# Kernel tuning notes

Hardware: AMD Instinct MI355X
Metric: run time of the kernel (lower is better)

The kernel has to match this reference:

```python
import jax, jax.numpy as jnp
import numpy as np

B, T, D = 2, 1024, 1024
H, DK = 16, 64  # n_head, d_k; inner dim = H*DK = D
INV_SQRT_DK = 1.0 / float(np.sqrt(DK))


def setup_inputs() -> dict:
    key = jax.random.key(0)
    ks = jax.random.split(key, 16)
    init = lambda k, shape: (jax.random.normal(k, shape, dtype=jnp.float32) * 0.02)
    return {
        "query": jax.random.normal(ks[0], (B, T, D), dtype=jnp.float32),
        "key": jax.random.normal(ks[1], (B, T, D), dtype=jnp.float32),
        "value": jax.random.normal(ks[2], (B, T, D), dtype=jnp.float32),
        "pos_k": jax.random.normal(ks[3], (T, T, DK), dtype=jnp.float32),
        "pos_v": jax.random.normal(ks[4], (T, T, DK), dtype=jnp.float32),
        "mask": jnp.ones((B, T, T), dtype=jnp.int32),
        "relative_attention_bias": jax.random.normal(ks[5], (1, H, T, T), dtype=jnp.float32),
        "Wq": init(ks[6], (D, D)), "bq": init(ks[7], (D,)),
        "Wk": init(ks[8], (D, D)), "bk": init(ks[9], (D,)),
        "Wv": init(ks[10], (D, D)), "bv": init(ks[11], (D,)),
        "Wo": init(ks[12], (D, D)), "bo": init(ks[13], (D,)),
    }


def reference(query, key, value, pos_k, pos_v, mask, relative_attention_bias,
              Wq, bq, Wk, bk, Wv, bv, Wo, bo):
    nb = query.shape[0]
    # projections -> (B, H, T, DK); q pre-scaled by 1/sqrt(d_k)
    q = (query @ Wq + bq).reshape(nb, -1, H, DK).transpose(0, 2, 1, 3) * INV_SQRT_DK
    k = (key @ Wk + bk).reshape(nb, -1, H, DK).transpose(0, 2, 1, 3)
    v = (value @ Wv + bv).reshape(nb, -1, H, DK).transpose(0, 2, 1, 3)

    # content scores + relative-position key scores (B, H, T, S)
    A = jnp.einsum('bhtd,bhsd->bhts', q, k)
    Bp = jnp.einsum('bhtd,tsd->bhts', q, pos_k)
    scores = A + Bp + relative_attention_bias

    # masked softmax: mask (B, T, S) -> invalid where mask == 0
    inv = (mask[:, None, :, :] == 0)  # (B, 1, T, S)
    scores = jnp.where(inv, -jnp.inf, scores)
    attn = jax.nn.softmax(scores, axis=-1)
    attn = jnp.where(inv, 0.0, attn)

    # value aggregation + relative-position value term
    x = jnp.einsum('bhts,bhsd->bhtd', attn, v)
    x = x + jnp.einsum('bhts,tsd->bhtd', attn, pos_v)

    x = x.transpose(0, 2, 1, 3).reshape(nb, -1, H * DK)  # (B, T, D)
    return x @ Wo + bo
```

## Files before the change

kernel.cpp:

```cpp
#include <hip/hip_runtime.h>


#define DEV __device__ __forceinline__

typedef short bf16x8 __attribute__((ext_vector_type(8)));
typedef float f32x4 __attribute__((ext_vector_type(4)));

DEV short f2b(float f) {
  unsigned u = __builtin_bit_cast(unsigned, f);
  u = (u + 0x7FFFu + ((u >> 16) & 1u)) >> 16;
  return (short)u;
}
DEV float b2f(short s) {
  unsigned u = ((unsigned)(unsigned short)s) << 16;
  return __builtin_bit_cast(float, u);
}

#define MFMA(a, b, c) __builtin_amdgcn_mfma_f32_16x16x32_bf16(a, b, c, 0, 0, 0)

__global__ __launch_bounds__(256) void k_cvt3(
    const float* __restrict__ a, const float* __restrict__ b, const float* __restrict__ c,
    short* __restrict__ oa, short* __restrict__ ob, short* __restrict__ oc) {
  const float* src = blockIdx.y == 0 ? a : (blockIdx.y == 1 ? b : c);
  short* dst = blockIdx.y == 0 ? oa : (blockIdx.y == 1 ? ob : oc);
  size_t i = ((size_t)blockIdx.x * 256 + threadIdx.x) * 8;
  float4 p0 = *(const float4*)(src + i);
  float4 p1 = *(const float4*)(src + i + 4);
  bf16x8 o;
  o[0] = f2b(p0.x); o[1] = f2b(p0.y); o[2] = f2b(p0.z); o[3] = f2b(p0.w);
  o[4] = f2b(p1.x); o[5] = f2b(p1.y); o[6] = f2b(p1.z); o[7] = f2b(p1.w);
  *(bf16x8*)(dst + i) = o;
}

__global__ __launch_bounds__(256) void k_wtrans4(
    const float* __restrict__ w0, const float* __restrict__ w1,
    const float* __restrict__ w2, const float* __restrict__ w3,
    short* __restrict__ o0, short* __restrict__ o1,
    short* __restrict__ o2, short* __restrict__ o3) {
  const float* src; short* dst;
  switch (blockIdx.z) {
    case 0: src = w0; dst = o0; break;
    case 1: src = w1; dst = o1; break;
    case 2: src = w2; dst = o2; break;
    default: src = w3; dst = o3;
  }
  __shared__ short LW[64][74];
  const int tid = threadIdx.x;
  const int k0 = blockIdx.y * 64, n0 = blockIdx.x * 64;
  {
    int c4 = (tid & 15) * 4;
#pragma unroll
    for (int i = 0; i < 4; ++i) {
      int r = (tid >> 4) + i * 16;
      float4 v = *(const float4*)(src + (size_t)(k0 + r) * 1024 + n0 + c4);
      LW[r][c4 + 0] = f2b(v.x); LW[r][c4 + 1] = f2b(v.y);
      LW[r][c4 + 2] = f2b(v.z); LW[r][c4 + 3] = f2b(v.w);
    }
  }
  __syncthreads();
  {
    int n = tid >> 2, kb = (tid & 3) * 16;
#pragma unroll
    for (int j2 = 0; j2 < 2; ++j2) {
      int kk = kb + j2 * 8;
      bf16x8 o;
#pragma unroll
      for (int j = 0; j < 8; ++j) o[j] = LW[kk + j][n];
      *(bf16x8*)(dst + (size_t)(n0 + n) * 1024 + k0 + kk) = o;
    }
  }
}

__global__ __launch_bounds__(256) void k_proj(
    const short* __restrict__ A, const short* __restrict__ WT,
    const float* __restrict__ bias, short* __restrict__ out, float scale) {
  __shared__ short As[64][40];
  __shared__ short Bs[64][40];
  const int n0 = blockIdx.x * 64, m0 = blockIdx.y * 64;
  const int tid = threadIdx.x;
  const int w = tid >> 6, l = tid & 63, lg = l >> 4, lr = l & 15;
  const int wm = (w >> 1) * 2, wn = (w & 1) * 2;
  const int sr = tid >> 2, sc = (tid & 3) * 8;
  f32x4 acc[2][2] = {};
  for (int k0 = 0; k0 < 1024; k0 += 32) {
    *(bf16x8*)&As[sr][sc] = *(const bf16x8*)(A + (size_t)(m0 + sr) * 1024 + k0 + sc);
    *(bf16x8*)&Bs[sr][sc] = *(const bf16x8*)(WT + (size_t)(n0 + sr) * 1024 + k0 + sc);
    __syncthreads();
    bf16x8 af[2], bfr[2];
#pragma unroll
    for (int mi = 0; mi < 2; ++mi) af[mi] = *(const bf16x8*)&As[(wm + mi) * 16 + lr][lg * 8];
#pragma unroll
    for (int ni = 0; ni < 2; ++ni) bfr[ni] = *(const bf16x8*)&Bs[(wn + ni) * 16 + lr][lg * 8];
#pragma unroll
    for (int mi = 0; mi < 2; ++mi)
#pragma unroll
      for (int ni = 0; ni < 2; ++ni) acc[mi][ni] = MFMA(af[mi], bfr[ni], acc[mi][ni]);
    __syncthreads();
  }
#pragma unroll
  for (int mi = 0; mi < 2; ++mi)
#pragma unroll
    for (int ni = 0; ni < 2; ++ni)
#pragma unroll
      for (int r = 0; r < 4; ++r) {
        int m = m0 + (wm + mi) * 16 + lg * 4 + r;
        int n = n0 + (wn + ni) * 16 + lr;
        float val = (acc[mi][ni][r] + bias[n]) * scale;
        int b = m >> 10, t = m & 1023, h = n >> 6, dk = n & 63;
        out[((size_t)(b * 16 + h) * 1024 + t) * 64 + dk] = f2b(val);
      }
}

__global__ __launch_bounds__(256) void k_projT(
    const short* __restrict__ A, const short* __restrict__ WT,
    const float* __restrict__ bias, short* __restrict__ out) {
  __shared__ short As[64][40];
  __shared__ short Bs[64][40];
  const int n0 = blockIdx.x * 64, m0 = blockIdx.y * 64;
  const int tid = threadIdx.x;
  const int w = tid >> 6, l = tid & 63, lg = l >> 4, lr = l & 15;
  const int wm = (w >> 1) * 2, wn = (w & 1) * 2;
  const int sr = tid >> 2, sc = (tid & 3) * 8;
  f32x4 acc[2][2] = {};
  for (int k0 = 0; k0 < 1024; k0 += 32) {
    *(bf16x8*)&As[sr][sc] = *(const bf16x8*)(A + (size_t)(m0 + sr) * 1024 + k0 + sc);
    *(bf16x8*)&Bs[sr][sc] = *(const bf16x8*)(WT + (size_t)(n0 + sr) * 1024 + k0 + sc);
    __syncthreads();
    bf16x8 af[2], bfr[2];
#pragma unroll
    for (int mi = 0; mi < 2; ++mi) af[mi] = *(const bf16x8*)&As[(wm + mi) * 16 + lr][lg * 8];
#pragma unroll
    for (int ni = 0; ni < 2; ++ni) bfr[ni] = *(const bf16x8*)&Bs[(wn + ni) * 16 + lr][lg * 8];
#pragma unroll
    for (int mi = 0; mi < 2; ++mi)
#pragma unroll
      for (int ni = 0; ni < 2; ++ni) acc[mi][ni] = MFMA(af[mi], bfr[ni], acc[mi][ni]);
    __syncthreads();
  }
#pragma unroll
  for (int mi = 0; mi < 2; ++mi)
#pragma unroll
    for (int ni = 0; ni < 2; ++ni)
#pragma unroll
      for (int r = 0; r < 4; ++r) {
        int m = m0 + (wm + mi) * 16 + lg * 4 + r;
        int n = n0 + (wn + ni) * 16 + lr;
        float val = acc[mi][ni][r] + bias[n];
        int b = m >> 10, t = m & 1023, h = n >> 6, dk = n & 63;
        out[(((size_t)(b * 16 + h) * 64 + dk) << 10) + t] = f2b(val);
      }
}

__global__ __launch_bounds__(256) void k_posk_bias(
    const short* __restrict__ q, const float* __restrict__ pos_k,
    const float* __restrict__ rab, const int* __restrict__ mask,
    short* __restrict__ S) {
  const int t = blockIdx.y;
  const int tid = threadIdx.x;
  const int w = tid >> 6, l = tid & 63, lg = l >> 4, lr = l & 15;
  const int s0 = blockIdx.x * 256 + w * 64;
  __shared__ short LW[4][32][74];
  bf16x8 af[2][2];
#pragma unroll
  for (int mi = 0; mi < 2; ++mi)
#pragma unroll
    for (int kk = 0; kk < 2; ++kk) {
      int bh = mi * 16 + lr;
      af[mi][kk] = *(const bf16x8*)(q + ((size_t)bh * 1024 + t) * 64 + kk * 32 + lg * 8);
    }
  f32x4 acc[2][4] = {};
#pragma unroll
  for (int ni = 0; ni < 4; ++ni) {
    int s = s0 + ni * 16 + lr;
#pragma unroll
    for (int kk = 0; kk < 2; ++kk) {
      const float* pk = pos_k + ((size_t)t * 1024 + s) * 64 + kk * 32 + lg * 8;
      const float4 p0 = *(const float4*)pk;
      const float4 p1 = *(const float4*)(pk + 4);
      bf16x8 bfr;
      bfr[0] = f2b(p0.x); bfr[1] = f2b(p0.y); bfr[2] = f2b(p0.z); bfr[3] = f2b(p0.w);
      bfr[4] = f2b(p1.x); bfr[5] = f2b(p1.y); bfr[6] = f2b(p1.z); bfr[7] = f2b(p1.w);
#pragma unroll
      for (int mi = 0; mi < 2; ++mi) acc[mi][ni] = MFMA(af[mi][kk], bfr, acc[mi][ni]);
    }
  }
#pragma unroll
  for (int ni = 0; ni < 4; ++ni) {
    int s = s0 + ni * 16 + lr;
    int msk0 = mask[(size_t)t * 1024 + s];
    int msk1 = mask[(size_t)(1024 + t) * 1024 + s];
#pragma unroll
    for (int r = 0; r < 4; ++r) {
      int h = lg * 4 + r;
      float bv = rab[((size_t)h * 1024 + t) * 1024 + s];
      float v0 = acc[0][ni][r] + bv;
      float v1 = acc[1][ni][r] + bv;
      if (msk0 == 0) v0 = -1e30f;
      if (msk1 == 0) v1 = -1e30f;
      LW[w][h][ni * 16 + lr] = f2b(v0);
      LW[w][16 + h][ni * 16 + lr] = f2b(v1);
    }
  }
#pragma unroll
  for (int rr = 0; rr < 4; ++rr) {
    int row = (l >> 3) + rr * 8;
    int s8 = (l & 7) * 8;
    bf16x8 o = *(const bf16x8*)&LW[w][row][s8];
    *(bf16x8*)(S + ((size_t)row * 1024 + t) * 1024 + s0 + s8) = o;
  }
}

__global__ __launch_bounds__(512, 4) void k_attn_softmax(
    const short* __restrict__ q, const short* __restrict__ kmat,
    short* __restrict__ S) {
  const int bh = blockIdx.y;
  const int tid = threadIdx.x;
  const int w = tid >> 6, l = tid & 63, lg = l >> 4, lr = l & 15;
  const int wm = w >> 2, wn = w & 3;
  const int t0 = blockIdx.x * 32 + wm * 16;
  const int scol = wn * 256;
  __shared__ short LS[8][16][266];
  __shared__ float redA[32][4];
  __shared__ float redB[32][4];

  short* sb = (short*)(S + ((size_t)bh * 1024 + t0) * 1024 + scol);
  const int r2 = l >> 5, c16 = (l & 31) * 8;
#pragma unroll
  for (int rr = 0; rr < 8; ++rr) {
    int row = rr * 2 + r2;
    *(bf16x8*)&LS[w][row][c16] = *(const bf16x8*)(sb + (size_t)row * 1024 + c16);
  }

  bf16x8 af[2];
#pragma unroll
  for (int kk = 0; kk < 2; ++kk)
    af[kk] = *(const bf16x8*)(q + ((size_t)bh * 1024 + (t0 + lr)) * 64 + kk * 32 + lg * 8);

  f32x4 acc[16];
#pragma unroll
  for (int ni = 0; ni < 16; ++ni) {
    int s = scol + ni * 16 + lr;
    const short* kp = kmat + ((size_t)bh * 1024 + s) * 64 + lg * 8;
    bf16x8 b0 = *(const bf16x8*)kp;
    bf16x8 b1 = *(const bf16x8*)(kp + 32);
    f32x4 a = {};
    a = MFMA(af[0], b0, a);
    a = MFMA(af[1], b1, a);
    acc[ni] = a;
  }
#pragma unroll
  for (int ni = 0; ni < 16; ++ni)
#pragma unroll
    for (int r = 0; r < 4; ++r) acc[ni][r] += b2f(LS[w][lg * 4 + r][ni * 16 + lr]);

  float pm[4];
#pragma unroll
  for (int r = 0; r < 4; ++r) {
    float m = acc[0][r];
#pragma unroll
    for (int ni = 1; ni < 16; ++ni) m = fmaxf(m, acc[ni][r]);
    m = fmaxf(m, __shfl_xor(m, 1));
    m = fmaxf(m, __shfl_xor(m, 2));
    m = fmaxf(m, __shfl_xor(m, 4));
    m = fmaxf(m, __shfl_xor(m, 8));
    pm[r] = m;
  }
  if (lr == 0) {
#pragma unroll
    for (int r = 0; r < 4; ++r) redA[wm * 16 + lg * 4 + r][wn] = pm[r];
  }
  __syncthreads();
  float rowm[4];
#pragma unroll
  for (int r = 0; r < 4; ++r) {
    int row = wm * 16 + lg * 4 + r;
    rowm[r] = fmaxf(fmaxf(redA[row][0], redA[row][1]), fmaxf(redA[row][2], redA[row][3]));
  }
  float rs[4];
#pragma unroll
  for (int r = 0; r < 4; ++r) {
    float sum = 0.f;
#pragma unroll
    for (int ni = 0; ni < 16; ++ni) {
      float e = __expf(acc[ni][r] - rowm[r]);
      acc[ni][r] = e;
      sum += e;
    }
    sum += __shfl_xor(sum, 1);
    sum += __shfl_xor(sum, 2);
    sum += __shfl_xor(sum, 4);
    sum += __shfl_xor(sum, 8);
    rs[r] = sum;
  }
  if (lr == 0) {
#pragma unroll
    for (int r = 0; r < 4; ++r) redB[wm * 16 + lg * 4 + r][wn] = rs[r];
  }
  __syncthreads();
#pragma unroll
  for (int r = 0; r < 4; ++r) {
    int row = wm * 16 + lg * 4 + r;
    float inv = 1.0f / (redB[row][0] + redB[row][1] + redB[row][2] + redB[row][3]);
#pragma unroll
    for (int ni = 0; ni < 16; ++ni) LS[w][lg * 4 + r][ni * 16 + lr] = f2b(acc[ni][r] * inv);
  }
#pragma unroll
  for (int rr = 0; rr < 8; ++rr) {
    int row = rr * 2 + r2;
    bf16x8 o = *(const bf16x8*)&LS[w][row][c16];
    *(bf16x8*)(sb + (size_t)row * 1024 + c16) = o;
  }
}

__global__ __launch_bounds__(256) void k_posv(
    const short* __restrict__ S, const float* __restrict__ pos_v,
    short* __restrict__ X0h) {
  const int t = blockIdx.x;
  const int tid = threadIdx.x;
  const int w = tid >> 6, l = tid & 63, lg = l >> 4, lr = l & 15;
  const int mi = w >> 1;
  const int nb = (w & 1) * 2;
  __shared__ short pv[256][66];
  f32x4 acc[2] = {};
  const int srow = tid >> 4;
  const int dk4 = (tid & 15) * 4;
  for (int c = 0; c < 4; ++c) {
    int sc = c * 256;
    if (c) __syncthreads();
#pragma unroll
    for (int it = 0; it < 16; ++it) {
      int s = srow + it * 16;
      float4 p = *(const float4*)(pos_v + ((size_t)t * 1024 + sc + s) * 64 + dk4);
      unsigned p0 = (unsigned)(unsigned short)f2b(p.x) | ((unsigned)(unsigned short)f2b(p.y) << 16);
      unsigned p1 = (unsigned)(unsigned short)f2b(p.z) | ((unsigned)(unsigned short)f2b(p.w) << 16);
      *(unsigned*)&pv[s][dk4] = p0;
      *(unsigned*)&pv[s][dk4 + 2] = p1;
    }
    __syncthreads();
    const int bh = mi * 16 + lr;
#pragma unroll
    for (int kk = 0; kk < 8; ++kk) {
      bf16x8 afr = *(const bf16x8*)(S + ((size_t)bh * 1024 + t) * 1024 + sc + kk * 32 + lg * 8);
#pragma unroll
      for (int ni = 0; ni < 2; ++ni) {
        int dk = (nb + ni) * 16 + lr;
        bf16x8 bfr;
#pragma unroll
        for (int j = 0; j < 8; ++j) bfr[j] = pv[kk * 32 + lg * 8 + j][dk];
        acc[ni] = MFMA(afr, bfr, acc[ni]);
      }
    }
  }
#pragma unroll
  for (int ni = 0; ni < 2; ++ni)
#pragma unroll
    for (int r = 0; r < 4; ++r) {
      int bh = mi * 16 + lg * 4 + r;
      int b = bh >> 4, h = bh & 15;
      int dk = (nb + ni) * 16 + lr;
      X0h[((size_t)(b * 1024 + t)) * 1024 + h * 64 + dk] = f2b(acc[ni][r]);
    }
}

__global__ __launch_bounds__(256) void k_av(
    const short* __restrict__ S, const short* __restrict__ vT,
    const short* __restrict__ X0h, short* __restrict__ X) {
  const int bh = blockIdx.y;
  const int tt0 = blockIdx.x * 128;
  const int tid = threadIdx.x;
  const int w = tid >> 6, l = tid & 63, lg = l >> 4, lr = l & 15;
  const short* vbase = vT + ((size_t)bh << 16);
  const short* sbase = S + ((size_t)bh << 20);
  f32x4 acc[2][4] = {};
#pragma unroll 4
  for (int kk = 0; kk < 32; ++kk) {
    bf16x8 afr[2];
#pragma unroll
    for (int mi = 0; mi < 2; ++mi) {
      int tt = tt0 + (w * 2 + mi) * 16 + lr;
      afr[mi] = *(const bf16x8*)(sbase + ((size_t)tt << 10) + kk * 32 + lg * 8);
    }
#pragma unroll
    for (int ni = 0; ni < 4; ++ni) {
      bf16x8 bfr = *(const bf16x8*)(vbase + ((ni * 16 + lr) << 10) + kk * 32 + lg * 8);
#pragma unroll
      for (int mi = 0; mi < 2; ++mi) acc[mi][ni] = MFMA(afr[mi], bfr, acc[mi][ni]);
    }
  }
  const int b = bh >> 4, h = bh & 15;
#pragma unroll
  for (int mi = 0; mi < 2; ++mi)
#pragma unroll
    for (int ni = 0; ni < 4; ++ni)
#pragma unroll
      for (int r = 0; r < 4; ++r) {
        int tt = tt0 + (w * 2 + mi) * 16 + lg * 4 + r;
        int d = h * 64 + ni * 16 + lr;
        size_t idx = ((size_t)(b * 1024 + tt)) * 1024 + d;
        X[idx] = f2b(b2f(X0h[idx]) + acc[mi][ni][r]);
      }
}

__global__ __launch_bounds__(256) void k_oproj(
    const short* __restrict__ X, const short* __restrict__ WT,
    const float* __restrict__ bias, float* __restrict__ out) {
  __shared__ short As[64][40];
  __shared__ short Bs[64][40];
  const int n0 = blockIdx.x * 64, m0 = blockIdx.y * 64;
  const int tid = threadIdx.x;
  const int w = tid >> 6, l = tid & 63, lg = l >> 4, lr = l & 15;
  const int wm = (w >> 1) * 2, wn = (w & 1) * 2;
  const int sr = tid >> 2, sc = (tid & 3) * 8;
  f32x4 acc[2][2] = {};
  for (int k0 = 0; k0 < 1024; k0 += 32) {
    *(bf16x8*)&As[sr][sc] = *(const bf16x8*)(X + (size_t)(m0 + sr) * 1024 + k0 + sc);
    *(bf16x8*)&Bs[sr][sc] = *(const bf16x8*)(WT + (size_t)(n0 + sr) * 1024 + k0 + sc);
    __syncthreads();
    bf16x8 af[2], bfr[2];
#pragma unroll
    for (int mi = 0; mi < 2; ++mi) af[mi] = *(const bf16x8*)&As[(wm + mi) * 16 + lr][lg * 8];
#pragma unroll
    for (int ni = 0; ni < 2; ++ni) bfr[ni] = *(const bf16x8*)&Bs[(wn + ni) * 16 + lr][lg * 8];
#pragma unroll
    for (int mi = 0; mi < 2; ++mi)
#pragma unroll
      for (int ni = 0; ni < 2; ++ni) acc[mi][ni] = MFMA(af[mi], bfr[ni], acc[mi][ni]);
    __syncthreads();
  }
#pragma unroll
  for (int mi = 0; mi < 2; ++mi)
#pragma unroll
    for (int ni = 0; ni < 2; ++ni)
#pragma unroll
      for (int r = 0; r < 4; ++r) {
        int m = m0 + (wm + mi) * 16 + lg * 4 + r;
        int n = n0 + (wn + ni) * 16 + lr;
        out[(size_t)m * 1024 + n] = acc[mi][ni][r] + bias[n];
      }
}

extern "C" void kernel_launch(void* const* d_in, const int* in_sizes, int n_in,
                              void* d_out, int out_size, void* d_ws, size_t ws_size,
                              hipStream_t stream) {
  (void)in_sizes; (void)n_in; (void)out_size; (void)ws_size;
  const float* query = (const float*)d_in[0];
  const float* key   = (const float*)d_in[1];
  const float* value = (const float*)d_in[2];
  const float* pos_k = (const float*)d_in[3];
  const float* pos_v = (const float*)d_in[4];
  const int*   mask  = (const int*)d_in[5];
  const float* rab   = (const float*)d_in[6];
  const float* Wq = (const float*)d_in[7];
  const float* bq = (const float*)d_in[8];
  const float* Wk = (const float*)d_in[9];
  const float* bk = (const float*)d_in[10];
  const float* Wv = (const float*)d_in[11];
  const float* bv = (const float*)d_in[12];
  const float* Wo = (const float*)d_in[13];
  const float* bo = (const float*)d_in[14];
  float* out = (float*)d_out;

  const size_t M2 = 2ull * 1024 * 1024;
  short* q   = (short*)d_ws;
  short* k   = q + M2;
  short* vT  = k + M2;
  short* S   = vT + M2;
  short* X0h = S + 32ull * 1024 * 1024;
  short* X   = X0h + M2;
  short* qin = X + M2;
  short* kin = qin + M2;
  short* vin = kin + M2;
  short* WqT = vin + M2;
  short* WkT = WqT + 1024 * 1024;
  short* WvT = WkT + 1024 * 1024;
  short* WoT = WvT + 1024 * 1024;

  k_cvt3<<<dim3(1024, 3), dim3(256), 0, stream>>>(query, key, value, qin, kin, vin);
  k_wtrans4<<<dim3(16, 16, 4), dim3(256), 0, stream>>>(Wq, Wk, Wv, Wo, WqT, WkT, WvT, WoT);
  k_proj<<<dim3(16, 32), dim3(256), 0, stream>>>(qin, WqT, bq, q, 0.125f);
  k_proj<<<dim3(16, 32), dim3(256), 0, stream>>>(kin, WkT, bk, k, 1.0f);
  k_projT<<<dim3(16, 32), dim3(256), 0, stream>>>(vin, WvT, bv, vT);
  k_posk_bias<<<dim3(4, 1024), dim3(256), 0, stream>>>(q, pos_k, rab, mask, S);
  k_attn_softmax<<<dim3(32, 32), dim3(512), 0, stream>>>(q, k, S);
  k_posv<<<dim3(1024), dim3(256), 0, stream>>>(S, pos_v, X0h);
  k_av<<<dim3(8, 32), dim3(256), 0, stream>>>(S, vT, X0h, X);
  k_oproj<<<dim3(16, 32), dim3(256), 0, stream>>>(X, WoT, bo, out);
}
```

Measured before the change: 319.3 us.

## Fuse Q/K/V projections into one 128x128-tile GEMM with direct-to-LDS loads

Merges the three projection launches into a single grid that picks the Q, K or V segment per block row, relying on qin/kin/vin and the transposed weights sitting contiguously in the workspace. Output and projection GEMMs move from 64x64 to 128x128 tiles with 4x4 MFMA fragments per wave, and load through global_load_lds instead of register staging. Epilogues stage results in LDS so the q/k and transposed v writes are coalesced 16-byte stores. The risks are the implicit layout dependency, fewer blocks for the output projection, and LDS reads without padding that may hit bank conflicts.

```diff
diff --git a/kernel.cpp b/kernel.cpp
--- a/kernel.cpp
+++ b/kernel.cpp
@@ -17,6 +17,12 @@
 }
 
 #define MFMA(a, b, c) __builtin_amdgcn_mfma_f32_16x16x32_bf16(a, b, c, 0, 0, 0)
+
+DEV void gload16(const void* g, void* l) {
+  __builtin_amdgcn_global_load_lds(
+      (const __attribute__((address_space(1))) void*)g,
+      (__attribute__((address_space(3))) void*)l, 16, 0, 0);
+}
 
 __global__ __launch_bounds__(256) void k_cvt3(
     const float* __restrict__ a, const float* __restrict__ b, const float* __restrict__ c,
@@ -71,84 +77,83 @@
   }
 }
 
-__global__ __launch_bounds__(256) void k_proj(
-    const short* __restrict__ A, const short* __restrict__ WT,
-    const float* __restrict__ bias, short* __restrict__ out, float scale) {
-  __shared__ short As[64][40];
-  __shared__ short Bs[64][40];
-  const int n0 = blockIdx.x * 64, m0 = blockIdx.y * 64;
+__global__ __launch_bounds__(256) void k_qkv(
+    const short* __restrict__ Ain, const short* __restrict__ WT,
+    const float* __restrict__ bq, const float* __restrict__ bk,
+    const float* __restrict__ bv,
+    short* __restrict__ qo, short* __restrict__ ko, short* __restrict__ vTo) {
+  __shared__ short As[128 * 32];
+  __shared__ short Bs[128 * 32];
+  __shared__ short LW[128][136];
   const int tid = threadIdx.x;
   const int w = tid >> 6, l = tid & 63, lg = l >> 4, lr = l & 15;
-  const int wm = (w >> 1) * 2, wn = (w & 1) * 2;
-  const int sr = tid >> 2, sc = (tid & 3) * 8;
-  f32x4 acc[2][2] = {};
+  const int wm = w >> 1, wn = w & 1;
+  const int n0 = blockIdx.x * 128;
+  const int m0 = blockIdx.y * 128;
+  const int seg = m0 >> 11;
+  const int mseg = m0 & 2047;
+  const short* Abase = Ain + ((size_t)m0 << 10);
+  const short* Bbase = WT + ((size_t)seg << 20) + ((size_t)n0 << 10);
+  const int srow = l >> 2, scol8 = (l & 3) * 8;
+  f32x4 acc[4][4] = {};
   for (int k0 = 0; k0 < 1024; k0 += 32) {
-    *(bf16x8*)&As[sr][sc] = *(const bf16x8*)(A + (size_t)(m0 + sr) * 1024 + k0 + sc);
-    *(bf16x8*)&Bs[sr][sc] = *(const bf16x8*)(WT + (size_t)(n0 + sr) * 1024 + k0 + sc);
+#pragma unroll
+    for (int c = 0; c < 2; ++c) {
+      int chunk = w * 2 + c;
+      int row = chunk * 16 + srow;
+      gload16(Abase + (size_t)row * 1024 + k0 + scol8, &As[chunk * 512]);
+      gload16(Bbase + (size_t)row * 1024 + k0 + scol8, &Bs[chunk * 512]);
+    }
     __syncthreads();
-    bf16x8 af[2], bfr[2];
-#pragma unroll
-    for (int mi = 0; mi < 2; ++mi) af[mi] = *(const bf16x8*)&As[(wm + mi) * 16 + lr][lg * 8];
-#pragma unroll
-    for (int ni = 0; ni < 2; ++ni) bfr[ni] = *(const bf16x8*)&Bs[(wn + ni) * 16 + lr][lg * 8];
-#pragma unroll
-    for (int mi = 0; mi < 2; ++mi)
-#pragma unroll
-      for (int ni = 0; ni < 2; ++ni) acc[mi][ni] = MFMA(af[mi], bfr[ni], acc[mi][ni]);
+    bf16x8 af[4], bf[4];
+#pragma unroll
+    for (int i = 0; i < 4; ++i) af[i] = *(const bf16x8*)&As[(wm * 64 + i * 16 + lr) * 32 + lg * 8];
+#pragma unroll
+    for (int i = 0; i < 4; ++i) bf[i] = *(const bf16x8*)&Bs[(wn * 64 + i * 16 + lr) * 32 + lg * 8];
+#pragma unroll
+    for (int mi = 0; mi < 4; ++mi)
+#pragma unroll
+      for (int ni = 0; ni < 4; ++ni) acc[mi][ni] = MFMA(af[mi], bf[ni], acc[mi][ni]);
     __syncthreads();
   }
-#pragma unroll
-  for (int mi = 0; mi < 2; ++mi)
-#pragma unroll
-    for (int ni = 0; ni < 2; ++ni)
-#pragma unroll
-      for (int r = 0; r < 4; ++r) {
-        int m = m0 + (wm + mi) * 16 + lg * 4 + r;
-        int n = n0 + (wn + ni) * 16 + lr;
-        float val = (acc[mi][ni][r] + bias[n]) * scale;
-        int b = m >> 10, t = m & 1023, h = n >> 6, dk = n & 63;
-        out[((size_t)(b * 16 + h) * 1024 + t) * 64 + dk] = f2b(val);
-      }
-}
-
-__global__ __launch_bounds__(256) void k_projT(
-    const short* __restrict__ A, const short* __restrict__ WT,
-    const float* __restrict__ bias, short* __restrict__ out) {
-  __shared__ short As[64][40];
-  __shared__ short Bs[64][40];
-  const int n0 = blockIdx.x * 64, m0 = blockIdx.y * 64;
-  const int tid = threadIdx.x;
-  const int w = tid >> 6, l = tid & 63, lg = l >> 4, lr = l & 15;
-  const int wm = (w >> 1) * 2, wn = (w & 1) * 2;
-  const int sr = tid >> 2, sc = (tid & 3) * 8;
-  f32x4 acc[2][2] = {};
-  for (int k0 = 0; k0 < 1024; k0 += 32) {
-    *(bf16x8*)&As[sr][sc] = *(const bf16x8*)(A + (size_t)(m0 + sr) * 1024 + k0 + sc);
-    *(bf16x8*)&Bs[sr][sc] = *(const bf16x8*)(WT + (size_t)(n0 + sr) * 1024 + k0 + sc);
-    __syncthreads();
-    bf16x8 af[2], bfr[2];
-#pragma unroll
-    for (int mi = 0; mi < 2; ++mi) af[mi] = *(const bf16x8*)&As[(wm + mi) * 16 + lr][lg * 8];
-#pragma unroll
-    for (int ni = 0; ni < 2; ++ni) bfr[ni] = *(const bf16x8*)&Bs[(wn + ni) * 16 + lr][lg * 8];
-#pragma unroll
-    for (int mi = 0; mi < 2; ++mi)
-#pragma unroll
-      for (int ni = 0; ni < 2; ++ni) acc[mi][ni] = MFMA(af[mi], bfr[ni], acc[mi][ni]);
-    __syncthreads();
-  }
-#pragma unroll
-  for (int mi = 0; mi < 2; ++mi)
-#pragma unroll
-    for (int ni = 0; ni < 2; ++ni)
-#pragma unroll
-      for (int r = 0; r < 4; ++r) {
-        int m = m0 + (wm + mi) * 16 + lg * 4 + r;
-        int n = n0 + (wn + ni) * 16 + lr;
-        float val = acc[mi][ni][r] + bias[n];
-        int b = m >> 10, t = m & 1023, h = n >> 6, dk = n & 63;
-        out[(((size_t)(b * 16 + h) * 64 + dk) << 10) + t] = f2b(val);
-      }
+  const float* bias = seg == 0 ? bq : (seg == 1 ? bk : bv);
+  const float scale = seg == 0 ? 0.125f : 1.0f;
+  float bvals[4];
+#pragma unroll
+  for (int ni = 0; ni < 4; ++ni) bvals[ni] = bias[n0 + wn * 64 + ni * 16 + lr];
+#pragma unroll
+  for (int mi = 0; mi < 4; ++mi)
+#pragma unroll
+    for (int ni = 0; ni < 4; ++ni)
+#pragma unroll
+      for (int r = 0; r < 4; ++r)
+        LW[wm * 64 + mi * 16 + lg * 4 + r][wn * 64 + ni * 16 + lr] =
+            f2b((acc[mi][ni][r] + bvals[ni]) * scale);
+  __syncthreads();
+  if (seg < 2) {
+    short* dst = seg == 0 ? qo : ko;
+    int r = tid >> 1, half = tid & 1;
+    int m = mseg + r, b = m >> 10, t = m & 1023;
+#pragma unroll
+    for (int g = 0; g < 8; ++g) {
+      int n = n0 + half * 64 + g * 8;
+      int h = n >> 6, dk = n & 63;
+      bf16x8 o = *(const bf16x8*)&LW[r][half * 64 + g * 8];
+      *(bf16x8*)(dst + (((size_t)(b * 16 + h) * 1024 + t) << 6) + dk) = o;
+    }
+  } else {
+    int dkc = tid & 127, th = tid >> 7;
+    int n = n0 + dkc, h = n >> 6, dk = n & 63;
+    int b = mseg >> 10;
+    int tbase = (mseg & 1023) + th * 64;
+#pragma unroll
+    for (int g = 0; g < 8; ++g) {
+      bf16x8 o;
+#pragma unroll
+      for (int e = 0; e < 8; ++e) o[e] = LW[th * 64 + g * 8 + e][dkc];
+      *(bf16x8*)(vTo + (((size_t)(b * 16 + h) * 64 + dk) << 10) + tbase + g * 8) = o;
+    }
+  }
 }
 
 __global__ __launch_bounds__(256) void k_posk_bias(
@@ -404,38 +409,49 @@
 __global__ __launch_bounds__(256) void k_oproj(
     const short* __restrict__ X, const short* __restrict__ WT,
     const float* __restrict__ bias, float* __restrict__ out) {
-  __shared__ short As[64][40];
-  __shared__ short Bs[64][40];
-  const int n0 = blockIdx.x * 64, m0 = blockIdx.y * 64;
+  __shared__ short As[128 * 32];
+  __shared__ short Bs[128 * 32];
   const int tid = threadIdx.x;
   const int w = tid >> 6, l = tid & 63, lg = l >> 4, lr = l & 15;
-  const int wm = (w >> 1) * 2, wn = (w & 1) * 2;
-  const int sr = tid >> 2, sc = (tid & 3) * 8;
-  f32x4 acc[2][2] = {};
+  const int wm = w >> 1, wn = w & 1;
+  const int n0 = blockIdx.x * 128;
+  const int m0 = blockIdx.y * 128;
+  const short* Abase = X + ((size_t)m0 << 10);
+  const short* Bbase = WT + ((size_t)n0 << 10);
+  const int srow = l >> 2, scol8 = (l & 3) * 8;
+  f32x4 acc[4][4] = {};
   for (int k0 = 0; k0 < 1024; k0 += 32) {
-    *(bf16x8*)&As[sr][sc] = *(const bf16x8*)(X + (size_t)(m0 + sr) * 1024 + k0 + sc);
-    *(bf16x8*)&Bs[sr][sc] = *(const bf16x8*)(WT + (size_t)(n0 + sr) * 1024 + k0 + sc);
+#pragma unroll
+    for (int c = 0; c < 2; ++c) {
+      int chunk = w * 2 + c;
+      int row = chunk * 16 + srow;
+      gload16(Abase + (size_t)row * 1024 + k0 + scol8, &As[chunk * 512]);
+      gload16(Bbase + (size_t)row * 1024 + k0 + scol8, &Bs[chunk * 512]);
+    }
     __syncthreads();
-    bf16x8 af[2], bfr[2];
-#pragma unroll
-    for (int mi = 0; mi < 2; ++mi) af[mi] = *(const bf16x8*)&As[(wm + mi) * 16 + lr][lg * 8];
-#pragma unroll
-    for (int ni = 0; ni < 2; ++ni) bfr[ni] = *(const bf16x8*)&Bs[(wn + ni) * 16 + lr][lg * 8];
-#pragma unroll
-    for (int mi = 0; mi < 2; ++mi)
-#pragma unroll
-      for (int ni = 0; ni < 2; ++ni) acc[mi][ni] = MFMA(af[mi], bfr[ni], acc[mi][ni]);
+    bf16x8 af[4], bf[4];
+#pragma unroll
+    for (int i = 0; i < 4; ++i) af[i] = *(const bf16x8*)&As[(wm * 64 + i * 16 + lr) * 32 + lg * 8];
+#pragma unroll
+    for (int i = 0; i < 4; ++i) bf[i] = *(const bf16x8*)&Bs[(wn * 64 + i * 16 + lr) * 32 + lg * 8];
+#pragma unroll
+    for (int mi = 0; mi < 4; ++mi)
+#pragma unroll
+      for (int ni = 0; ni < 4; ++ni) acc[mi][ni] = MFMA(af[mi], bf[ni], acc[mi][ni]);
     __syncthreads();
   }
-#pragma unroll
-  for (int mi = 0; mi < 2; ++mi)
-#pragma unroll
-    for (int ni = 0; ni < 2; ++ni)
+  float bvals[4];
+#pragma unroll
+  for (int ni = 0; ni < 4; ++ni) bvals[ni] = bias[n0 + wn * 64 + ni * 16 + lr];
+#pragma unroll
+  for (int mi = 0; mi < 4; ++mi)
+#pragma unroll
+    for (int ni = 0; ni < 4; ++ni)
 #pragma unroll
       for (int r = 0; r < 4; ++r) {
-        int m = m0 + (wm + mi) * 16 + lg * 4 + r;
-        int n = n0 + (wn + ni) * 16 + lr;
-        out[(size_t)m * 1024 + n] = acc[mi][ni][r] + bias[n];
+        int m = m0 + wm * 64 + mi * 16 + lg * 4 + r;
+        int n = n0 + wn * 64 + ni * 16 + lr;
+        out[(size_t)m * 1024 + n] = acc[mi][ni][r] + bvals[ni];
       }
 }
 
@@ -477,12 +493,10 @@
 
   k_cvt3<<<dim3(1024, 3), dim3(256), 0, stream>>>(query, key, value, qin, kin, vin);
   k_wtrans4<<<dim3(16, 16, 4), dim3(256), 0, stream>>>(Wq, Wk, Wv, Wo, WqT, WkT, WvT, WoT);
-  k_proj<<<dim3(16, 32), dim3(256), 0, stream>>>(qin, WqT, bq, q, 0.125f);
-  k_proj<<<dim3(16, 32), dim3(256), 0, stream>>>(kin, WkT, bk, k, 1.0f);
-  k_projT<<<dim3(16, 32), dim3(256), 0, stream>>>(vin, WvT, bv, vT);
+  k_qkv<<<dim3(8, 48), dim3(256), 0, stream>>>(qin, WqT, bq, bk, bv, q, k, vT);
   k_posk_bias<<<dim3(4, 1024), dim3(256), 0, stream>>>(q, pos_k, rab, mask, S);
   k_attn_softmax<<<dim3(32, 32), dim3(512), 0, stream>>>(q, k, S);
   k_posv<<<dim3(1024), dim3(256), 0, stream>>>(S, pos_v, X0h);
   k_av<<<dim3(8, 32), dim3(256), 0, stream>>>(S, vT, X0h, X);
-  k_oproj<<<dim3(16, 32), dim3(256), 0, stream>>>(X, WoT, bo, out);
-}
+  k_oproj<<<dim3(8, 16), dim3(256), 0, stream>>>(X, WoT, bo, out);
+}
```

New measurement: 307.1 us (median of 2 runs). 3.8% less time.
